# Performance work log

Hardware: AMD Instinct MI355X
Metric: run time of the kernel (lower is better)

The kernel has to match this reference:

```python
import jax, jax.numpy as jnp
import numpy as np

B, C, H, N, M = 8, 256, 4, 2048, 2048
D = C // H  # head_dim = 64
EPS = 1e-5


def conv1d(x, W, b):
    # 1x1 Conv1d == per-position GEMM: x [B, Cin, N], W [Cout, Cin], b [Cout]
    return jnp.einsum('oi,bin->bon', W, x) + b[:, None]


def setup_inputs() -> dict:
    key = jax.random.key(0)
    ks = jax.random.split(key, 16)
    s = 1.0 / np.sqrt(C)
    s2 = 1.0 / np.sqrt(2 * C)
    return {
        'desc1': jax.random.normal(ks[0], (B, C, N), jnp.float32),
        'desc2': jax.random.normal(ks[1], (B, C, M), jnp.float32),
        'weight_v': jax.random.uniform(ks[2], (B, M), jnp.float32),
        'Wq': jax.random.normal(ks[3], (C, C), jnp.float32) * s,
        'bq': jnp.zeros((C,), jnp.float32),
        'Wk': jax.random.normal(ks[4], (C, C), jnp.float32) * s,
        'bk': jnp.zeros((C,), jnp.float32),
        'Wv': jax.random.normal(ks[5], (C, C), jnp.float32) * s,
        'bv': jnp.zeros((C,), jnp.float32),
        'Wm': jax.random.normal(ks[6], (C, C), jnp.float32) * s,
        'bm': jnp.zeros((C,), jnp.float32),
        'Wc1': jax.random.normal(ks[7], (2 * C, 2 * C), jnp.float32) * s2,
        'bc1': jnp.zeros((2 * C,), jnp.float32),
        'bn_gamma': jnp.ones((2 * C,), jnp.float32),
        'bn_beta': jnp.zeros((2 * C,), jnp.float32),
        'bn_mean': jnp.zeros((2 * C,), jnp.float32),
        'bn_var': jnp.ones((2 * C,), jnp.float32),
        'Wc2': jax.random.normal(ks[8], (C, 2 * C), jnp.float32) * s2,
        'bc2': jnp.zeros((C,), jnp.float32),
    }


def reference(desc1, desc2, weight_v, Wq, bq, Wk, bk, Wv, bv, Wm, bm,
              Wc1, bc1, bn_gamma, bn_beta, bn_mean, bn_var, Wc2, bc2):
    b = desc1.shape[0]
    # projections -> [B, H, D, N/M]
    q = conv1d(desc1, Wq, bq).reshape(b, H, D, -1)
    k = conv1d(desc2, Wk, bk).reshape(b, H, D, -1)
    v = conv1d(desc2, Wv, bv).reshape(b, H, D, -1)
    v = v * weight_v[:, None, None, :]
    score = jax.nn.softmax(jnp.einsum('bhdn,bhdm->bhnm', q, k) / jnp.sqrt(jnp.asarray(D, q.dtype)), axis=-1)
    add_value = jnp.einsum('bhnm,bhdm->bhdn', score, v).reshape(b, H * D, -1)
    add_value = conv1d(add_value, Wm, bm)
    cat = jnp.concatenate([desc1, add_value], axis=1)  # [B, 2C, N]
    h = conv1d(cat, Wc1, bc1)
    # BatchNorm (inference, running stats)
    inv = bn_gamma / jnp.sqrt(bn_var + EPS)
    h = jax.nn.relu(h * inv[:, None] + (bn_beta - bn_mean * inv)[:, None])
    return desc1 + conv1d(h, Wc2, bc2)
```

## Files before the change

kernel.cpp:

```cpp
#include <hip/hip_runtime.h>
#include <hip/hip_bf16.h>
#include <math.h>

constexpr int Bb = 8;
constexpr int Cc = 256;
constexpr int Hh = 4;
constexpr int Nn = 2048;
constexpr int Mm = 2048;
constexpr size_t BCN = (size_t)Bb * Cc * Nn;

typedef __attribute__((ext_vector_type(8))) short short8;
typedef __attribute__((ext_vector_type(4))) float f32x4;

__device__ __forceinline__ unsigned short bfu(float x) {
  __hip_bfloat16 b = __float2bfloat16(x);
  return __builtin_bit_cast(unsigned short, b);
}

__device__ __forceinline__ void gload16(const unsigned short* g, unsigned short* l) {
  __builtin_amdgcn_global_load_lds(
      (const __attribute__((address_space(1))) unsigned int*)g,
      (__attribute__((address_space(3))) unsigned int*)l, 16, 0, 0);
}

__global__ __launch_bounds__(256) void quantw_kernel(
    const float* __restrict__ s0, const float* __restrict__ s1,
    const float* __restrict__ s2, const float* __restrict__ s3,
    const float* __restrict__ s4, const float* __restrict__ s5,
    unsigned short* __restrict__ d0, unsigned short* __restrict__ d1,
    unsigned short* __restrict__ d2, unsigned short* __restrict__ d3,
    unsigned short* __restrict__ d4, unsigned short* __restrict__ d5)
{
  const int seg = blockIdx.y;
  const float* s; unsigned short* d; int cnt; float sc = 1.f;
  switch (seg) {
    case 0: s = s0; d = d0; cnt = 65536;  sc = 0.125f; break;
    case 1: s = s1; d = d1; cnt = 65536;  break;
    case 2: s = s2; d = d2; cnt = 65536;  break;
    case 3: s = s3; d = d3; cnt = 65536;  break;
    case 4: s = s4; d = d4; cnt = 262144; break;
    default: s = s5; d = d5; cnt = 131072; break;
  }
  for (int i = blockIdx.x * 256 + threadIdx.x; i < cnt / 4; i += 64 * 256) {
    float4 v = ((const float4*)s)[i];
    unsigned int lo = bfu(v.x * sc) | ((unsigned int)bfu(v.y * sc) << 16);
    unsigned int hi = bfu(v.z * sc) | ((unsigned int)bfu(v.w * sc) << 16);
    ((uint2*)d)[i] = make_uint2(lo, hi);
  }
}

__global__ __launch_bounds__(256) void trans_kernel(
    const float* __restrict__ S1, const float* __restrict__ S2,
    unsigned short* __restrict__ D1, unsigned short* __restrict__ D2)
{
  __shared__ float T[64][65];
  const int z = blockIdx.z, b = z & 7;
  const float* S = (z >> 3) ? S2 : S1;
  unsigned short* D = (z >> 3) ? D2 : D1;
  const int n0 = blockIdx.x * 64, c0 = blockIdx.y * 64;
  const int t = threadIdx.x, t4 = t >> 6, tl = t & 63;

  #pragma unroll
  for (int r = 0; r < 16; ++r) {
    int cl = r * 4 + t4;
    T[cl][tl] = S[((size_t)b * 256 + c0 + cl) * 2048 + n0 + tl];
  }
  __syncthreads();
  #pragma unroll
  for (int r = 0; r < 16; ++r) {
    int nl = r * 4 + t4;
    D[((size_t)b * 2048 + n0 + nl) * 256 + c0 + tl] = bfu(T[tl][nl]);
  }
}

template<int K1, int K2, int COUT, int EPI>
__global__ __launch_bounds__(256) void gemm_kernel(
    const unsigned short* __restrict__ Wb,
    const unsigned short* __restrict__ X1, const unsigned short* __restrict__ X2,
    const float* __restrict__ bias,
    const float* __restrict__ p0, const float* __restrict__ p1,
    const float* __restrict__ p2, const float* __restrict__ p3,
    void* __restrict__ Yv, float oscale)
{
  constexpr int KT = K1 + K2;
  constexpr bool TRANS = (EPI == 0 || EPI == 2 || EPI == 3);
  __shared__ unsigned short lds[2 * 128 * 64];
  unsigned short* Wl = lds;
  unsigned short* Xl = lds + 128 * 64;

  const int t = threadIdx.x;
  const int w = t >> 6, l = t & 63;
  const int c = l & 15, h4 = l >> 4;
  const int n0 = blockIdx.x * 128;
  const int o0 = blockIdx.y * 128;
  const int b  = blockIdx.z;
  const int wo = (w & 1) * 64, wn = (w >> 1) * 64;

  const int r8  = t >> 3;
  const int kgx = (t & 7) ^ (r8 & 7);

  const unsigned short* Xb1 = X1 + (size_t)b * 2048 * K1;

  f32x4 acc[4][4] = {};

  #pragma unroll 1
  for (int kt = 0; kt < KT / 64; ++kt) {
    __syncthreads();
    #pragma unroll
    for (int q = 0; q < 4; ++q) {
      int row = q * 32 + r8;
      gload16(Wb + (size_t)(o0 + row) * KT + kt * 64 + kgx * 8,
              Wl + q * 2048 + w * 512);
      const unsigned short* src;
      if constexpr (K2 == 0) {
        src = Xb1 + (size_t)(n0 + row) * K1 + kt * 64 + kgx * 8;
      } else {
        src = (kt * 64 < K1)
          ? Xb1 + (size_t)(n0 + row) * K1 + kt * 64 + kgx * 8
          : X2 + ((size_t)b * 2048 + n0 + row) * K2 + (kt * 64 - K1) + kgx * 8;
      }
      gload16(src, Xl + q * 2048 + w * 512);
    }
    __syncthreads();

    #pragma unroll
    for (int kk = 0; kk < 2; ++kk) {
      short8 wf[4], xf[4];
      #pragma unroll
      for (int f = 0; f < 4; ++f) {
        int row = wo + f * 16 + c;
        wf[f] = *(const short8*)((const char*)Wl + row * 128 + (((kk * 4 + h4) ^ (row & 7)) << 4));
      }
      #pragma unroll
      for (int f = 0; f < 4; ++f) {
        int row = wn + f * 16 + c;
        xf[f] = *(const short8*)((const char*)Xl + row * 128 + (((kk * 4 + h4) ^ (row & 7)) << 4));
      }
      #pragma unroll
      for (int i = 0; i < 4; ++i)
        #pragma unroll
        for (int j = 0; j < 4; ++j) {
          if constexpr (TRANS)
            acc[i][j] = __builtin_amdgcn_mfma_f32_16x16x32_bf16(xf[i], wf[j], acc[i][j], 0, 0, 0);
          else
            acc[i][j] = __builtin_amdgcn_mfma_f32_16x16x32_bf16(wf[i], xf[j], acc[i][j], 0, 0, 0);
        }
    }
  }

  if constexpr (EPI == 0) {
    unsigned short* Y = (unsigned short*)Yv;
    #pragma unroll
    for (int j = 0; j < 4; ++j) {
      int og = o0 + wo + j * 16 + c;
      float bb = bias[og] * oscale;
      int hh = og >> 6, d = og & 63;
      unsigned short* Yp = Y + (((size_t)b * Hh + hh) * 2048) * 64 + d;
      #pragma unroll
      for (int i = 0; i < 4; ++i) {
        #pragma unroll
        for (int r = 0; r < 4; ++r) {
          int ng = n0 + wn + i * 16 + h4 * 4 + r;
          Yp[(size_t)ng * 64] = bfu(acc[i][j][r] + bb);
        }
      }
    }
  } else if constexpr (EPI == 2) {
    unsigned short* Y = (unsigned short*)Yv;
    #pragma unroll
    for (int j = 0; j < 4; ++j) {
      int og = o0 + wo + j * 16 + c;
      float bb = bias[og];
      #pragma unroll
      for (int i = 0; i < 4; ++i)
        #pragma unroll
        for (int r = 0; r < 4; ++r) {
          int ng = n0 + wn + i * 16 + h4 * 4 + r;
          Y[((size_t)b * 2048 + ng) * 256 + og] = bfu(acc[i][j][r] + bb);
        }
    }
  } else if constexpr (EPI == 3) {
    unsigned short* Y = (unsigned short*)Yv;
    #pragma unroll
    for (int j = 0; j < 4; ++j) {
      int og = o0 + wo + j * 16 + c;
      float bb  = bias[og];
      float inv = p0[og] / sqrtf(p3[og] + 1e-5f);
      float add = p1[og] - p2[og] * inv;
      #pragma unroll
      for (int i = 0; i < 4; ++i)
        #pragma unroll
        for (int r = 0; r < 4; ++r) {
          int ng = n0 + wn + i * 16 + h4 * 4 + r;
          float v = fmaxf((acc[i][j][r] + bb) * inv + add, 0.f);
          Y[((size_t)b * 2048 + ng) * 512 + og] = bfu(v);
        }
    }
  } else if constexpr (EPI == 1) {
    unsigned short* Y = (unsigned short*)Yv;
    #pragma unroll
    for (int j = 0; j < 4; ++j) {
      int mg = n0 + wn + j * 16 + c;
      float sc = p0[(size_t)b * 2048 + mg];
      #pragma unroll
      for (int i = 0; i < 4; ++i)
        #pragma unroll
        for (int r = 0; r < 4; ++r) {
          int og = o0 + wo + i * 16 + h4 * 4 + r;
          Y[((size_t)b * 256 + og) * 2048 + mg] = bfu((acc[i][j][r] + bias[og]) * sc);
        }
    }
  } else {
    float* Y = (float*)Yv;
    #pragma unroll
    for (int j = 0; j < 4; ++j) {
      int ng = n0 + wn + j * 16 + c;
      #pragma unroll
      for (int i = 0; i < 4; ++i)
        #pragma unroll
        for (int r = 0; r < 4; ++r) {
          int og = o0 + wo + i * 16 + h4 * 4 + r;
          size_t idx = ((size_t)b * 256 + og) * 2048 + ng;
          Y[idx] = acc[i][j][r] + bias[og] + p0[idx];
        }
    }
  }
}

__global__ __launch_bounds__(256) void attn_mfma_kernel(
    const unsigned short* __restrict__ Qt, const unsigned short* __restrict__ Kt,
    const unsigned short* __restrict__ Vb, unsigned short* __restrict__ Ot)
{
  const int id  = blockIdx.x;
  const int xcd = id & 7;
  const int s8  = id >> 3;
  const int bh  = xcd + 8 * (s8 >> 4);
  const int nb  = s8 & 15;
  const int wv  = threadIdx.x >> 6;
  const int l   = threadIdx.x & 63;
  const int c   = l & 15;
  const int h   = l >> 4;
  const int n0  = nb * 128 + wv * 32;

  const unsigned short* Qw = Qt + ((size_t)bh * Nn + n0) * 64;
  const unsigned short* Kb = Kt + (size_t)bh * Mm * 64;
  const unsigned short* Vw = Vb + (size_t)bh * 64 * Mm;

  __shared__ unsigned short Pl[4][32 * 64];
  char* P = (char*)Pl[wv];

  short8 qf[2][2];
  #pragma unroll
  for (int j = 0; j < 2; ++j)
    #pragma unroll
    for (int ks = 0; ks < 2; ++ks)
      qf[j][ks] = *(const short8*)(Qw + ((size_t)(j*16 + c)) * 64 + ks*32 + h*8);

  f32x4 acc[4][2];
  #pragma unroll
  for (int d = 0; d < 4; ++d)
    #pragma unroll
    for (int j = 0; j < 2; ++j) acc[d][j] = (f32x4){0.f,0.f,0.f,0.f};
  float rowM[2] = {-1e30f, -1e30f};
  float rowL[2] = {0.f, 0.f};

  #pragma unroll 1
  for (int m0 = 0; m0 < Mm; m0 += 64) {
    short8 kf[4][2];
    #pragma unroll
    for (int g = 0; g < 4; ++g)
      #pragma unroll
      for (int ks = 0; ks < 2; ++ks)
        kf[g][ks] = *(const short8*)(Kb + ((size_t)(m0 + g*16 + c)) * 64 + ks*32 + h*8);

    f32x4 sc4[4][2];
    #pragma unroll
    for (int g = 0; g < 4; ++g)
      #pragma unroll
      for (int j = 0; j < 2; ++j) {
        f32x4 z = (f32x4){0.f,0.f,0.f,0.f};
        z = __builtin_amdgcn_mfma_f32_16x16x32_bf16(kf[g][0], qf[j][0], z, 0, 0, 0);
        z = __builtin_amdgcn_mfma_f32_16x16x32_bf16(kf[g][1], qf[j][1], z, 0, 0, 0);
        sc4[g][j] = z;
      }

    short8 vf[4][2];
    #pragma unroll
    for (int db = 0; db < 4; ++db)
      #pragma unroll
      for (int ks = 0; ks < 2; ++ks)
        vf[db][ks] = *(const short8*)(Vw + ((size_t)(db*16 + c)) * Mm + m0 + ks*32 + h*8);

    #pragma unroll
    for (int j = 0; j < 2; ++j) {
      float mx = -1e30f;
      #pragma unroll
      for (int g = 0; g < 4; ++g)
        #pragma unroll
        for (int r = 0; r < 4; ++r) mx = fmaxf(mx, sc4[g][j][r]);
      mx = fmaxf(mx, __shfl_xor(mx, 16));
      mx = fmaxf(mx, __shfl_xor(mx, 32));
      float nm = fmaxf(rowM[j], mx);
      float corr = __expf(rowM[j] - nm);
      rowM[j] = nm;
      float sum = 0.f;
      #pragma unroll
      for (int g = 0; g < 4; ++g) {
        #pragma unroll
        for (int r = 0; r < 4; ++r) {
          float e = __expf(sc4[g][j][r] - nm);
          sc4[g][j][r] = e;
          sum += e;
        }
      }
      sum += __shfl_xor(sum, 16);
      sum += __shfl_xor(sum, 32);
      rowL[j] = rowL[j] * corr + sum;
      #pragma unroll
      for (int db = 0; db < 4; ++db)
        #pragma unroll
        for (int r = 0; r < 4; ++r) acc[db][j][r] *= corr;

      #pragma unroll
      for (int g = 0; g < 4; ++g) {
        unsigned int lo = ((unsigned int)bfu(sc4[g][j][1]) << 16) | bfu(sc4[g][j][0]);
        unsigned int hi = ((unsigned int)bfu(sc4[g][j][3]) << 16) | bfu(sc4[g][j][2]);
        int off = (j*16 + c) * 128 + g*32 + h*8;
        off ^= (c & 7) << 4;
        *(uint2*)(P + off) = make_uint2(lo, hi);
      }
    }

    #pragma unroll
    for (int j = 0; j < 2; ++j) {
      short8 pf[2];
      #pragma unroll
      for (int ks = 0; ks < 2; ++ks) {
        int off = (j*16 + c) * 128 + ks*64 + h*16;
        off ^= (c & 7) << 4;
        pf[ks] = *(const short8*)(P + off);
      }
      #pragma unroll
      for (int db = 0; db < 4; ++db) {
        acc[db][j] = __builtin_amdgcn_mfma_f32_16x16x32_bf16(vf[db][0], pf[0], acc[db][j], 0, 0, 0);
        acc[db][j] = __builtin_amdgcn_mfma_f32_16x16x32_bf16(vf[db][1], pf[1], acc[db][j], 0, 0, 0);
      }
    }
  }

  const float invl[2] = {1.f / rowL[0], 1.f / rowL[1]};
  unsigned short* Ob = Ot + ((size_t)(bh >> 2) * Nn) * 256 + (bh & 3) * 64;
  #pragma unroll
  for (int db = 0; db < 4; ++db)
    #pragma unroll
    for (int j = 0; j < 2; ++j) {
      unsigned int lo = ((unsigned int)bfu(acc[db][j][1] * invl[j]) << 16) | bfu(acc[db][j][0] * invl[j]);
      unsigned int hi = ((unsigned int)bfu(acc[db][j][3] * invl[j]) << 16) | bfu(acc[db][j][2] * invl[j]);
      *(uint2*)(Ob + (size_t)(n0 + j*16 + c) * 256 + db*16 + h*4) = make_uint2(lo, hi);
    }
}

extern "C" void kernel_launch(void* const* d_in, const int* in_sizes, int n_in,
                              void* d_out, int out_size, void* d_ws, size_t ws_size,
                              hipStream_t stream)
{
  (void)in_sizes; (void)n_in; (void)out_size; (void)ws_size;
  const float* desc1 = (const float*)d_in[0];
  const float* desc2 = (const float*)d_in[1];
  const float* wvv   = (const float*)d_in[2];
  const float* Wq  = (const float*)d_in[3];  const float* bq  = (const float*)d_in[4];
  const float* Wk  = (const float*)d_in[5];  const float* bk  = (const float*)d_in[6];
  const float* Wv  = (const float*)d_in[7];  const float* bv  = (const float*)d_in[8];
  const float* Wm  = (const float*)d_in[9];  const float* bm  = (const float*)d_in[10];
  const float* Wc1 = (const float*)d_in[11]; const float* bc1 = (const float*)d_in[12];
  const float* bng = (const float*)d_in[13]; const float* bnb = (const float*)d_in[14];
  const float* bnm = (const float*)d_in[15]; const float* bnv = (const float*)d_in[16];
  const float* Wc2 = (const float*)d_in[17]; const float* bc2 = (const float*)d_in[18];
  float* out = (float*)d_out;

  unsigned short* u = (unsigned short*)d_ws;
  unsigned short* D1t  = u;
  unsigned short* D2t  = u + BCN;
  unsigned short* Qt   = u + 2 * BCN;
  unsigned short* Kt   = u + 3 * BCN;
  unsigned short* Vbb  = u + 4 * BCN;
  unsigned short* Ot    = D2t;
  unsigned short* MoutT = Qt;
  unsigned short* HT    = Kt;
  unsigned short* Wqb  = u + 5 * BCN;
  unsigned short* Wkb  = Wqb + 65536;
  unsigned short* Wvb  = Wkb + 65536;
  unsigned short* Wmb  = Wvb + 65536;
  unsigned short* Wc1b = Wmb + 65536;
  unsigned short* Wc2b = Wc1b + 262144;

  dim3 blk(256);
  quantw_kernel<<<dim3(64, 6), blk, 0, stream>>>(
      Wq, Wk, Wv, Wm, Wc1, Wc2, Wqb, Wkb, Wvb, Wmb, Wc1b, Wc2b);
  trans_kernel<<<dim3(32, 4, 16), blk, 0, stream>>>(desc1, desc2, D1t, D2t);

  gemm_kernel<256,0,256,0><<<dim3(16, 2, Bb), blk, 0, stream>>>(
      Wqb, D1t, nullptr, bq, nullptr,nullptr,nullptr,nullptr, Qt, 0.125f);
  gemm_kernel<256,0,256,0><<<dim3(16, 2, Bb), blk, 0, stream>>>(
      Wkb, D2t, nullptr, bk, nullptr,nullptr,nullptr,nullptr, Kt, 1.0f);
  gemm_kernel<256,0,256,1><<<dim3(16, 2, Bb), blk, 0, stream>>>(
      Wvb, D2t, nullptr, bv, wvv,nullptr,nullptr,nullptr, Vbb, 1.0f);
  attn_mfma_kernel<<<dim3(512), blk, 0, stream>>>(Qt, Kt, Vbb, Ot);
  gemm_kernel<256,0,256,2><<<dim3(16, 2, Bb), blk, 0, stream>>>(
      Wmb, Ot, nullptr, bm, nullptr,nullptr,nullptr,nullptr, MoutT, 1.0f);
  gemm_kernel<256,256,512,3><<<dim3(16, 4, Bb), blk, 0, stream>>>(
      Wc1b, D1t, MoutT, bc1, bng,bnb,bnm,bnv, HT, 1.0f);
  gemm_kernel<512,0,256,4><<<dim3(16, 2, Bb), blk, 0, stream>>>(
      Wc2b, HT, nullptr, bc2, desc1,nullptr,nullptr,nullptr, out, 1.0f);
}
```

Before: 299.3 us.

## Halve query rows per wave in attention kernel to double grid and occupancy

```diff
diff --git a/kernel.cpp b/kernel.cpp
--- a/kernel.cpp
+++ b/kernel.cpp
@@ -157,13 +157,12 @@
       int hh = og >> 6, d = og & 63;
       unsigned short* Yp = Y + (((size_t)b * Hh + hh) * 2048) * 64 + d;
       #pragma unroll
-      for (int i = 0; i < 4; ++i) {
+      for (int i = 0; i < 4; ++i)
         #pragma unroll
         for (int r = 0; r < 4; ++r) {
           int ng = n0 + wn + i * 16 + h4 * 4 + r;
           Yp[(size_t)ng * 64] = bfu(acc[i][j][r] + bb);
         }
-      }
     }
   } else if constexpr (EPI == 2) {
     unsigned short* Y = (unsigned short*)Yv;
@@ -227,42 +226,37 @@
   }
 }
 
-__global__ __launch_bounds__(256) void attn_mfma_kernel(
+__global__ __launch_bounds__(256, 4) void attn_mfma_kernel(
     const unsigned short* __restrict__ Qt, const unsigned short* __restrict__ Kt,
     const unsigned short* __restrict__ Vb, unsigned short* __restrict__ Ot)
 {
   const int id  = blockIdx.x;
   const int xcd = id & 7;
   const int s8  = id >> 3;
-  const int bh  = xcd + 8 * (s8 >> 4);
-  const int nb  = s8 & 15;
+  const int bh  = xcd + 8 * (s8 >> 5);
+  const int nb  = s8 & 31;
   const int wv  = threadIdx.x >> 6;
   const int l   = threadIdx.x & 63;
   const int c   = l & 15;
   const int h   = l >> 4;
-  const int n0  = nb * 128 + wv * 32;
+  const int n0  = nb * 64 + wv * 16;
 
   const unsigned short* Qw = Qt + ((size_t)bh * Nn + n0) * 64;
   const unsigned short* Kb = Kt + (size_t)bh * Mm * 64;
   const unsigned short* Vw = Vb + (size_t)bh * 64 * Mm;
 
-  __shared__ unsigned short Pl[4][32 * 64];
+  __shared__ unsigned short Pl[4][16 * 64];
   char* P = (char*)Pl[wv];
 
-  short8 qf[2][2];
-  #pragma unroll
-  for (int j = 0; j < 2; ++j)
-    #pragma unroll
-    for (int ks = 0; ks < 2; ++ks)
-      qf[j][ks] = *(const short8*)(Qw + ((size_t)(j*16 + c)) * 64 + ks*32 + h*8);
-
-  f32x4 acc[4][2];
-  #pragma unroll
-  for (int d = 0; d < 4; ++d)
-    #pragma unroll
-    for (int j = 0; j < 2; ++j) acc[d][j] = (f32x4){0.f,0.f,0.f,0.f};
-  float rowM[2] = {-1e30f, -1e30f};
-  float rowL[2] = {0.f, 0.f};
+  short8 qf[2];
+  #pragma unroll
+  for (int ks = 0; ks < 2; ++ks)
+    qf[ks] = *(const short8*)(Qw + (size_t)c * 64 + ks * 32 + h * 8);
+
+  f32x4 acc[4];
+  #pragma unroll
+  for (int d = 0; d < 4; ++d) acc[d] = (f32x4){0.f, 0.f, 0.f, 0.f};
+  float rowM = -1e30f, rowL = 0.f;
 
   #pragma unroll 1
   for (int m0 = 0; m0 < Mm; m0 += 64) {
@@ -271,93 +265,80 @@
     for (int g = 0; g < 4; ++g)
       #pragma unroll
       for (int ks = 0; ks < 2; ++ks)
-        kf[g][ks] = *(const short8*)(Kb + ((size_t)(m0 + g*16 + c)) * 64 + ks*32 + h*8);
-
-    f32x4 sc4[4][2];
+        kf[g][ks] = *(const short8*)(Kb + ((size_t)(m0 + g * 16 + c)) * 64 + ks * 32 + h * 8);
+
+    f32x4 sc4[4];
+    #pragma unroll
+    for (int g = 0; g < 4; ++g) {
+      f32x4 z = (f32x4){0.f, 0.f, 0.f, 0.f};
+      z = __builtin_amdgcn_mfma_f32_16x16x32_bf16(kf[g][0], qf[0], z, 0, 0, 0);
+      z = __builtin_amdgcn_mfma_f32_16x16x32_bf16(kf[g][1], qf[1], z, 0, 0, 0);
+      sc4[g] = z;
+    }
+
+    short8 vf[4][2];
+    #pragma unroll
+    for (int db = 0; db < 4; ++db)
+      #pragma unroll
+      for (int ks = 0; ks < 2; ++ks)
+        vf[db][ks] = *(const short8*)(Vw + ((size_t)(db * 16 + c)) * Mm + m0 + ks * 32 + h * 8);
+
+    float mx = -1e30f;
     #pragma unroll
     for (int g = 0; g < 4; ++g)
       #pragma unroll
-      for (int j = 0; j < 2; ++j) {
-        f32x4 z = (f32x4){0.f,0.f,0.f,0.f};
-        z = __builtin_amdgcn_mfma_f32_16x16x32_bf16(kf[g][0], qf[j][0], z, 0, 0, 0);
-        z = __builtin_amdgcn_mfma_f32_16x16x32_bf16(kf[g][1], qf[j][1], z, 0, 0, 0);
-        sc4[g][j] = z;
+      for (int r = 0; r < 4; ++r) mx = fmaxf(mx, sc4[g][r]);
+    mx = fmaxf(mx, __shfl_xor(mx, 16));
+    mx = fmaxf(mx, __shfl_xor(mx, 32));
+    float nm = fmaxf(rowM, mx);
+    float corr = __expf(rowM - nm);
+    rowM = nm;
+    float sum = 0.f;
+    #pragma unroll
+    for (int g = 0; g < 4; ++g)
+      #pragma unroll
+      for (int r = 0; r < 4; ++r) {
+        float e = __expf(sc4[g][r] - nm);
+        sc4[g][r] = e;
+        sum += e;
       }
-
-    short8 vf[4][2];
+    sum += __shfl_xor(sum, 16);
+    sum += __shfl_xor(sum, 32);
+    rowL = rowL * corr + sum;
     #pragma unroll
     for (int db = 0; db < 4; ++db)
       #pragma unroll
-      for (int ks = 0; ks < 2; ++ks)
-        vf[db][ks] = *(const short8*)(Vw + ((size_t)(db*16 + c)) * Mm + m0 + ks*32 + h*8);
-
-    #pragma unroll
-    for (int j = 0; j < 2; ++j) {
-      float mx = -1e30f;
-      #pragma unroll
-      for (int g = 0; g < 4; ++g)
-        #pragma unroll
-        for (int r = 0; r < 4; ++r) mx = fmaxf(mx, sc4[g][j][r]);
-      mx = fmaxf(mx, __shfl_xor(mx, 16));
-      mx = fmaxf(mx, __shfl_xor(mx, 32));
-      float nm = fmaxf(rowM[j], mx);
-      float corr = __expf(rowM[j] - nm);
-      rowM[j] = nm;
-      float sum = 0.f;
-      #pragma unroll
-      for (int g = 0; g < 4; ++g) {
-        #pragma unroll
-        for (int r = 0; r < 4; ++r) {
-          float e = __expf(sc4[g][j][r] - nm);
-          sc4[g][j][r] = e;
-          sum += e;
-        }
-      }
-      sum += __shfl_xor(sum, 16);
-      sum += __shfl_xor(sum, 32);
-      rowL[j] = rowL[j] * corr + sum;
-      #pragma unroll
-      for (int db = 0; db < 4; ++db)
-        #pragma unroll
-        for (int r = 0; r < 4; ++r) acc[db][j][r] *= corr;
-
-      #pragma unroll
-      for (int g = 0; g < 4; ++g) {
-        unsigned int lo = ((unsigned int)bfu(sc4[g][j][1]) << 16) | bfu(sc4[g][j][0]);
-        unsigned int hi = ((unsigned int)bfu(sc4[g][j][3]) << 16) | bfu(sc4[g][j][2]);
-        int off = (j*16 + c) * 128 + g*32 + h*8;
-        off ^= (c & 7) << 4;
-        *(uint2*)(P + off) = make_uint2(lo, hi);
-      }
-    }
-
-    #pragma unroll
-    for (int j = 0; j < 2; ++j) {
-      short8 pf[2];
-      #pragma unroll
-      for (int ks = 0; ks < 2; ++ks) {
-        int off = (j*16 + c) * 128 + ks*64 + h*16;
-        off ^= (c & 7) << 4;
-        pf[ks] = *(const short8*)(P + off);
-      }
-      #pragma unroll
-      for (int db = 0; db < 4; ++db) {
-        acc[db][j] = __builtin_amdgcn_mfma_f32_16x16x32_bf16(vf[db][0], pf[0], acc[db][j], 0, 0, 0);
-        acc[db][j] = __builtin_amdgcn_mfma_f32_16x16x32_bf16(vf[db][1], pf[1], acc[db][j], 0, 0, 0);
-      }
-    }
-  }
-
-  const float invl[2] = {1.f / rowL[0], 1.f / rowL[1]};
+      for (int r = 0; r < 4; ++r) acc[db][r] *= corr;
+
+    #pragma unroll
+    for (int g = 0; g < 4; ++g) {
+      unsigned int lo = ((unsigned int)bfu(sc4[g][1]) << 16) | bfu(sc4[g][0]);
+      unsigned int hi = ((unsigned int)bfu(sc4[g][3]) << 16) | bfu(sc4[g][2]);
+      int off = c * 128 + ((g * 32 + h * 8) ^ ((c & 7) << 4));
+      *(uint2*)(P + off) = make_uint2(lo, hi);
+    }
+
+    short8 pf[2];
+    #pragma unroll
+    for (int ks = 0; ks < 2; ++ks) {
+      int off = c * 128 + ((ks * 64 + h * 16) ^ ((c & 7) << 4));
+      pf[ks] = *(const short8*)(P + off);
+    }
+    #pragma unroll
+    for (int db = 0; db < 4; ++db) {
+      acc[db] = __builtin_amdgcn_mfma_f32_16x16x32_bf16(vf[db][0], pf[0], acc[db], 0, 0, 0);
+      acc[db] = __builtin_amdgcn_mfma_f32_16x16x32_bf16(vf[db][1], pf[1], acc[db], 0, 0, 0);
+    }
+  }
+
+  const float invl = 1.f / rowL;
   unsigned short* Ob = Ot + ((size_t)(bh >> 2) * Nn) * 256 + (bh & 3) * 64;
   #pragma unroll
-  for (int db = 0; db < 4; ++db)
-    #pragma unroll
-    for (int j = 0; j < 2; ++j) {
-      unsigned int lo = ((unsigned int)bfu(acc[db][j][1] * invl[j]) << 16) | bfu(acc[db][j][0] * invl[j]);
-      unsigned int hi = ((unsigned int)bfu(acc[db][j][3] * invl[j]) << 16) | bfu(acc[db][j][2] * invl[j]);
-      *(uint2*)(Ob + (size_t)(n0 + j*16 + c) * 256 + db*16 + h*4) = make_uint2(lo, hi);
-    }
+  for (int db = 0; db < 4; ++db) {
+    unsigned int lo = ((unsigned int)bfu(acc[db][1] * invl) << 16) | bfu(acc[db][0] * invl);
+    unsigned int hi = ((unsigned int)bfu(acc[db][3] * invl) << 16) | bfu(acc[db][2] * invl);
+    *(uint2*)(Ob + (size_t)(n0 + c) * 256 + db * 16 + h * 4) = make_uint2(lo, hi);
+  }
 }
 
 extern "C" void kernel_launch(void* const* d_in, const int* in_sizes, int n_in,
@@ -405,7 +386,7 @@
       Wkb, D2t, nullptr, bk, nullptr,nullptr,nullptr,nullptr, Kt, 1.0f);
   gemm_kernel<256,0,256,1><<<dim3(16, 2, Bb), blk, 0, stream>>>(
       Wvb, D2t, nullptr, bv, wvv,nullptr,nullptr,nullptr, Vbb, 1.0f);
-  attn_mfma_kernel<<<dim3(512), blk, 0, stream>>>(Qt, Kt, Vbb, Ot);
+  attn_mfma_kernel<<<dim3(1024), blk, 0, stream>>>(Qt, Kt, Vbb, Ot);
   gemm_kernel<256,0,256,2><<<dim3(16, 2, Bb), blk, 0, stream>>>(
       Wmb, Ot, nullptr, bm, nullptr,nullptr,nullptr,nullptr, MoutT, 1.0f);
   gemm_kernel<256,256,512,3><<<dim3(16, 4, Bb), blk, 0, stream>>>(
```

Result: slower. 411.5 us (+37.5%).

## Fuse Q/K/V projections into one launch and double-buffer K loads in attention

Applied to the files above, without the earlier changes.

```diff
diff --git a/kernel.cpp b/kernel.cpp
--- a/kernel.cpp
+++ b/kernel.cpp
@@ -3,11 +3,10 @@
 #include <math.h>
 
 constexpr int Bb = 8;
-constexpr int Cc = 256;
 constexpr int Hh = 4;
 constexpr int Nn = 2048;
 constexpr int Mm = 2048;
-constexpr size_t BCN = (size_t)Bb * Cc * Nn;
+constexpr size_t BCN = (size_t)Bb * 256 * Nn;
 
 typedef __attribute__((ext_vector_type(8))) short short8;
 typedef __attribute__((ext_vector_type(4))) float f32x4;
@@ -73,6 +72,112 @@
   }
 }
 
+__global__ __launch_bounds__(256) void qkv_kernel(
+    const unsigned short* __restrict__ Wqb, const unsigned short* __restrict__ Wkb,
+    const unsigned short* __restrict__ Wvb,
+    const unsigned short* __restrict__ D1t, const unsigned short* __restrict__ D2t,
+    const float* __restrict__ bq, const float* __restrict__ bk,
+    const float* __restrict__ bv, const float* __restrict__ wvv,
+    unsigned short* __restrict__ Qt, unsigned short* __restrict__ Kt,
+    unsigned short* __restrict__ Vbb)
+{
+  constexpr int KT = 256;
+  __shared__ unsigned short lds[2 * 128 * 64];
+  unsigned short* Wl = lds;
+  unsigned short* Xl = lds + 128 * 64;
+
+  const int mode = blockIdx.z >> 3;
+  const int b    = blockIdx.z & 7;
+  const unsigned short* Wb = mode == 0 ? Wqb : (mode == 1 ? Wkb : Wvb);
+  const unsigned short* X  = mode == 0 ? D1t : D2t;
+  const float* bias        = mode == 0 ? bq  : (mode == 1 ? bk  : bv);
+
+  const int t = threadIdx.x;
+  const int w = t >> 6, l = t & 63;
+  const int c = l & 15, h4 = l >> 4;
+  const int n0 = blockIdx.x * 128;
+  const int o0 = blockIdx.y * 128;
+  const int wo = (w & 1) * 64, wn = (w >> 1) * 64;
+  const int r8  = t >> 3;
+  const int kgx = (t & 7) ^ (r8 & 7);
+
+  const unsigned short* Xb = X + (size_t)b * 2048 * KT;
+
+  f32x4 acc[4][4] = {};
+
+  #pragma unroll 1
+  for (int kt = 0; kt < 4; ++kt) {
+    __syncthreads();
+    #pragma unroll
+    for (int q = 0; q < 4; ++q) {
+      int row = q * 32 + r8;
+      gload16(Wb + (size_t)(o0 + row) * KT + kt * 64 + kgx * 8, Wl + q * 2048 + w * 512);
+      gload16(Xb + (size_t)(n0 + row) * KT + kt * 64 + kgx * 8, Xl + q * 2048 + w * 512);
+    }
+    __syncthreads();
+
+    #pragma unroll
+    for (int kk = 0; kk < 2; ++kk) {
+      short8 wf[4], xf[4];
+      #pragma unroll
+      for (int f = 0; f < 4; ++f) {
+        int row = wo + f * 16 + c;
+        wf[f] = *(const short8*)((const char*)Wl + row * 128 + (((kk * 4 + h4) ^ (row & 7)) << 4));
+      }
+      #pragma unroll
+      for (int f = 0; f < 4; ++f) {
+        int row = wn + f * 16 + c;
+        xf[f] = *(const short8*)((const char*)Xl + row * 128 + (((kk * 4 + h4) ^ (row & 7)) << 4));
+      }
+      if (mode != 2) {
+        #pragma unroll
+        for (int i = 0; i < 4; ++i)
+          #pragma unroll
+          for (int j = 0; j < 4; ++j)
+            acc[i][j] = __builtin_amdgcn_mfma_f32_16x16x32_bf16(xf[i], wf[j], acc[i][j], 0, 0, 0);
+      } else {
+        #pragma unroll
+        for (int i = 0; i < 4; ++i)
+          #pragma unroll
+          for (int j = 0; j < 4; ++j)
+            acc[i][j] = __builtin_amdgcn_mfma_f32_16x16x32_bf16(wf[i], xf[j], acc[i][j], 0, 0, 0);
+      }
+    }
+  }
+
+  if (mode != 2) {
+    float os = mode == 0 ? 0.125f : 1.0f;
+    unsigned short* Y = mode == 0 ? Qt : Kt;
+    #pragma unroll
+    for (int j = 0; j < 4; ++j) {
+      int og = o0 + wo + j * 16 + c;
+      float bb = bias[og] * os;
+      int hh = og >> 6, d = og & 63;
+      unsigned short* Yp = Y + (((size_t)b * Hh + hh) * 2048) * 64 + d;
+      #pragma unroll
+      for (int i = 0; i < 4; ++i)
+        #pragma unroll
+        for (int r = 0; r < 4; ++r) {
+          int ng = n0 + wn + i * 16 + h4 * 4 + r;
+          Yp[(size_t)ng * 64] = bfu(acc[i][j][r] + bb);
+        }
+    }
+  } else {
+    #pragma unroll
+    for (int j = 0; j < 4; ++j) {
+      int mg = n0 + wn + j * 16 + c;
+      float sc = wvv[(size_t)b * 2048 + mg];
+      #pragma unroll
+      for (int i = 0; i < 4; ++i)
+        #pragma unroll
+        for (int r = 0; r < 4; ++r) {
+          int og = o0 + wo + i * 16 + h4 * 4 + r;
+          Vbb[((size_t)b * 256 + og) * 2048 + mg] = bfu((acc[i][j][r] + bias[og]) * sc);
+        }
+    }
+  }
+}
+
 template<int K1, int K2, int COUT, int EPI>
 __global__ __launch_bounds__(256) void gemm_kernel(
     const unsigned short* __restrict__ Wb,
@@ -80,10 +185,10 @@
     const float* __restrict__ bias,
     const float* __restrict__ p0, const float* __restrict__ p1,
     const float* __restrict__ p2, const float* __restrict__ p3,
-    void* __restrict__ Yv, float oscale)
+    void* __restrict__ Yv)
 {
   constexpr int KT = K1 + K2;
-  constexpr bool TRANS = (EPI == 0 || EPI == 2 || EPI == 3);
+  constexpr bool TRANS = (EPI == 2 || EPI == 3);
   __shared__ unsigned short lds[2 * 128 * 64];
   unsigned short* Wl = lds;
   unsigned short* Xl = lds + 128 * 64;
@@ -148,24 +253,7 @@
     }
   }
 
-  if constexpr (EPI == 0) {
-    unsigned short* Y = (unsigned short*)Yv;
-    #pragma unroll
-    for (int j = 0; j < 4; ++j) {
-      int og = o0 + wo + j * 16 + c;
-      float bb = bias[og] * oscale;
-      int hh = og >> 6, d = og & 63;
-      unsigned short* Yp = Y + (((size_t)b * Hh + hh) * 2048) * 64 + d;
-      #pragma unroll
-      for (int i = 0; i < 4; ++i) {
-        #pragma unroll
-        for (int r = 0; r < 4; ++r) {
-          int ng = n0 + wn + i * 16 + h4 * 4 + r;
-          Yp[(size_t)ng * 64] = bfu(acc[i][j][r] + bb);
-        }
-      }
-    }
-  } else if constexpr (EPI == 2) {
+  if constexpr (EPI == 2) {
     unsigned short* Y = (unsigned short*)Yv;
     #pragma unroll
     for (int j = 0; j < 4; ++j) {
@@ -196,20 +284,6 @@
           Y[((size_t)b * 2048 + ng) * 512 + og] = bfu(v);
         }
     }
-  } else if constexpr (EPI == 1) {
-    unsigned short* Y = (unsigned short*)Yv;
-    #pragma unroll
-    for (int j = 0; j < 4; ++j) {
-      int mg = n0 + wn + j * 16 + c;
-      float sc = p0[(size_t)b * 2048 + mg];
-      #pragma unroll
-      for (int i = 0; i < 4; ++i)
-        #pragma unroll
-        for (int r = 0; r < 4; ++r) {
-          int og = o0 + wo + i * 16 + h4 * 4 + r;
-          Y[((size_t)b * 256 + og) * 2048 + mg] = bfu((acc[i][j][r] + bias[og]) * sc);
-        }
-    }
   } else {
     float* Y = (float*)Yv;
     #pragma unroll
@@ -228,7 +302,7 @@
 }
 
 __global__ __launch_bounds__(256) void attn_mfma_kernel(
-    const unsigned short* __restrict__ Qt, const unsigned short* __restrict__ Kt,
+    const unsigned short* __restrict__ Qt, const unsigned short* __restrict__ Ktp,
     const unsigned short* __restrict__ Vb, unsigned short* __restrict__ Ot)
 {
   const int id  = blockIdx.x;
@@ -243,7 +317,7 @@
   const int n0  = nb * 128 + wv * 32;
 
   const unsigned short* Qw = Qt + ((size_t)bh * Nn + n0) * 64;
-  const unsigned short* Kb = Kt + (size_t)bh * Mm * 64;
+  const unsigned short* Kb = Ktp + (size_t)bh * Mm * 64;
   const unsigned short* Vw = Vb + (size_t)bh * 64 * Mm;
 
   __shared__ unsigned short Pl[4][32 * 64];
@@ -264,16 +338,19 @@
   float rowM[2] = {-1e30f, -1e30f};
   float rowL[2] = {0.f, 0.f};
 
-  #pragma unroll 1
-  for (int m0 = 0; m0 < Mm; m0 += 64) {
-    short8 kf[4][2];
+  short8 kfA[4][2], kfB[4][2];
+
+  auto loadK = [&](short8 (&kf)[4][2], int m0) {
     #pragma unroll
     for (int g = 0; g < 4; ++g)
       #pragma unroll
       for (int ks = 0; ks < 2; ++ks)
         kf[g][ks] = *(const short8*)(Kb + ((size_t)(m0 + g*16 + c)) * 64 + ks*32 + h*8);
-
+  };
+
+  auto tile = [&](short8 (&kf)[4][2], int m0) {
     f32x4 sc4[4][2];
+    __builtin_amdgcn_s_setprio(1);
     #pragma unroll
     for (int g = 0; g < 4; ++g)
       #pragma unroll
@@ -283,6 +360,7 @@
         z = __builtin_amdgcn_mfma_f32_16x16x32_bf16(kf[g][1], qf[j][1], z, 0, 0, 0);
         sc4[g][j] = z;
       }
+    __builtin_amdgcn_s_setprio(0);
 
     short8 vf[4][2];
     #pragma unroll
@@ -305,14 +383,13 @@
       rowM[j] = nm;
       float sum = 0.f;
       #pragma unroll
-      for (int g = 0; g < 4; ++g) {
+      for (int g = 0; g < 4; ++g)
         #pragma unroll
         for (int r = 0; r < 4; ++r) {
           float e = __expf(sc4[g][j][r] - nm);
           sc4[g][j][r] = e;
           sum += e;
         }
-      }
       sum += __shfl_xor(sum, 16);
       sum += __shfl_xor(sum, 32);
       rowL[j] = rowL[j] * corr + sum;
@@ -340,12 +417,23 @@
         off ^= (c & 7) << 4;
         pf[ks] = *(const short8*)(P + off);
       }
+      __builtin_amdgcn_s_setprio(1);
       #pragma unroll
       for (int db = 0; db < 4; ++db) {
         acc[db][j] = __builtin_amdgcn_mfma_f32_16x16x32_bf16(vf[db][0], pf[0], acc[db][j], 0, 0, 0);
         acc[db][j] = __builtin_amdgcn_mfma_f32_16x16x32_bf16(vf[db][1], pf[1], acc[db][j], 0, 0, 0);
       }
-    }
+      __builtin_amdgcn_s_setprio(0);
+    }
+  };
+
+  loadK(kfA, 0);
+  #pragma unroll 1
+  for (int m0 = 0; m0 < Mm; m0 += 128) {
+    loadK(kfB, m0 + 64);
+    tile(kfA, m0);
+    loadK(kfA, (m0 + 128) & (Mm - 1));
+    tile(kfB, m0 + 64);
   }
 
   const float invl[2] = {1.f / rowL[0], 1.f / rowL[1]};
@@ -399,17 +487,13 @@
       Wq, Wk, Wv, Wm, Wc1, Wc2, Wqb, Wkb, Wvb, Wmb, Wc1b, Wc2b);
   trans_kernel<<<dim3(32, 4, 16), blk, 0, stream>>>(desc1, desc2, D1t, D2t);
 
-  gemm_kernel<256,0,256,0><<<dim3(16, 2, Bb), blk, 0, stream>>>(
-      Wqb, D1t, nullptr, bq, nullptr,nullptr,nullptr,nullptr, Qt, 0.125f);
-  gemm_kernel<256,0,256,0><<<dim3(16, 2, Bb), blk, 0, stream>>>(
-      Wkb, D2t, nullptr, bk, nullptr,nullptr,nullptr,nullptr, Kt, 1.0f);
-  gemm_kernel<256,0,256,1><<<dim3(16, 2, Bb), blk, 0, stream>>>(
-      Wvb, D2t, nullptr, bv, wvv,nullptr,nullptr,nullptr, Vbb, 1.0f);
+  qkv_kernel<<<dim3(16, 2, 24), blk, 0, stream>>>(
+      Wqb, Wkb, Wvb, D1t, D2t, bq, bk, bv, wvv, Qt, Kt, Vbb);
   attn_mfma_kernel<<<dim3(512), blk, 0, stream>>>(Qt, Kt, Vbb, Ot);
   gemm_kernel<256,0,256,2><<<dim3(16, 2, Bb), blk, 0, stream>>>(
-      Wmb, Ot, nullptr, bm, nullptr,nullptr,nullptr,nullptr, MoutT, 1.0f);
+      Wmb, Ot, nullptr, bm, nullptr,nullptr,nullptr,nullptr, MoutT);
   gemm_kernel<256,256,512,3><<<dim3(16, 4, Bb), blk, 0, stream>>>(
-      Wc1b, D1t, MoutT, bc1, bng,bnb,bnm,bnv, HT, 1.0f);
+      Wc1b, D1t, MoutT, bc1, bng,bnb,bnm,bnv, HT);
   gemm_kernel<512,0,256,4><<<dim3(16, 2, Bb), blk, 0, stream>>>(
-      Wc2b, HT, nullptr, bc2, desc1,nullptr,nullptr,nullptr, out, 1.0f);
-}
+      Wc2b, HT, nullptr, bc2, desc1,nullptr,nullptr,nullptr, out);
+}
```

After: 298.4 us. No clear change (-0.3%).
